# Performance work log

Measured on AMD Instinct MI355X. Metric: run time of the kernel, lower is better.

Reference implementation:

```python
import jax, jax.numpy as jnp
import numpy as np

B, S, D, H = 2, 2048, 2048, 16
DEPTH = D // H


def setup_inputs() -> dict:
    key = jax.random.key(0)
    ks = jax.random.split(key, 12)
    std = 1.0 / np.sqrt(D)
    mk = lambda k, shape: (jax.random.uniform(k, shape, jnp.float32) * 2 - 1) * std
    # causal additive mask: 1.0 where future position (masked), 0.0 elsewhere
    mask = jnp.triu(jnp.ones((S, S), jnp.float32), k=1)[None, None]
    return {
        "q": jax.random.normal(ks[0], (B, S, D), jnp.float32),
        "k": jax.random.normal(ks[1], (B, S, D), jnp.float32),
        "v": jax.random.normal(ks[2], (B, S, D), jnp.float32),
        "mask": mask,
        "wq_w": mk(ks[3], (D, D)), "wq_b": mk(ks[4], (D,)),
        "wk_w": mk(ks[5], (D, D)), "wk_b": mk(ks[6], (D,)),
        "wv_w": mk(ks[7], (D, D)), "wv_b": mk(ks[8], (D,)),
        "dense_w": mk(ks[9], (D, D)), "dense_b": mk(ks[10], (D,)),
    }


def split_heads(x):
    # [B,S,D] -> [B,H,S,depth]
    b, s, _ = x.shape
    return x.reshape(b, s, H, DEPTH).transpose(0, 2, 1, 3)


def reference(q, k, v, mask, wq_w, wq_b, wk_w, wk_b, wv_w, wv_b, dense_w, dense_b):
    # torch Linear: y = x @ W.T + b
    qh = split_heads(q @ wq_w.T + wq_b)
    kh = split_heads(k @ wk_w.T + wk_b)
    vh = split_heads(v @ wv_w.T + wv_b)
    scale = 1.0 / jnp.sqrt(jnp.asarray(DEPTH, jnp.float32))
    logits = jnp.einsum("bhqd,bhkd->bhqk", qh, kh) * scale
    logits = logits + mask * (-1e9)
    weights = jax.nn.softmax(logits, axis=-1)  # dropout is identity in eval
    out = jnp.einsum("bhqk,bhkd->bhqd", weights, vh)
    out = out.transpose(0, 2, 1, 3).reshape(q.shape[0], -1, D)
    return out @ dense_w.T + dense_b
```

## Files before the change

kernel.cpp:

```cpp
#include <hip/hip_runtime.h>
#include <hip/hip_bf16.h>


typedef __bf16 bf16x8 __attribute__((ext_vector_type(8)));
typedef float f32x4 __attribute__((ext_vector_type(4)));
typedef float f32x16 __attribute__((ext_vector_type(16)));
typedef unsigned short u16;
typedef unsigned int u32;

#define DEV static __device__ __forceinline__

DEV void gload_lds16(const void* g, void* l) {
  __builtin_amdgcn_global_load_lds(
      (const __attribute__((address_space(1))) void*)g,
      (__attribute__((address_space(3))) void*)l, 16, 0, 0);
}

DEV f32x4 mfma16(bf16x8 a, bf16x8 b, f32x4 c) {
  return __builtin_amdgcn_mfma_f32_16x16x32_bf16(a, b, c, 0, 0, 0);
}

DEV f32x16 mfma32(bf16x8 a, bf16x8 b, f32x16 c) {
  return __builtin_amdgcn_mfma_f32_32x32x16_bf16(a, b, c, 0, 0, 0);
}

DEV u16 f2bf(float x) {
  return __builtin_bit_cast(u16, __float2bfloat16(x));
}

DEV u32 pack2(float lo, float hi_) {
  return (u32)f2bf(lo) | ((u32)f2bf(hi_) << 16);
}

#define BAR() __builtin_amdgcn_s_barrier()

__global__ void __launch_bounds__(256) conv_f32_bf16(
    const float* __restrict__ in, u16* __restrict__ out) {
  const size_t i = ((size_t)blockIdx.x * 256 + threadIdx.x) * 4;
  const float4 v = *reinterpret_cast<const float4*>(in + i);
  ushort4 o;
  o.x = f2bf(v.x); o.y = f2bf(v.y); o.z = f2bf(v.z); o.w = f2bf(v.w);
  *reinterpret_cast<ushort4*>(out + i) = o;
}

__global__ void __launch_bounds__(256) conv_all(
    const float* __restrict__ s0, const float* __restrict__ s1,
    const float* __restrict__ s2, const float* __restrict__ s3,
    const float* __restrict__ s4, const float* __restrict__ s5,
    const float* __restrict__ s6,
    u16* __restrict__ d0, u16* __restrict__ d1, u16* __restrict__ d2,
    u16* __restrict__ d3, u16* __restrict__ d4, u16* __restrict__ d5,
    u16* __restrict__ d6, const size_t nact, const size_t nw) {
  const int j = blockIdx.y;
  const size_t i = ((size_t)blockIdx.x * 256 + threadIdx.x) * 4;
  const float* s; u16* d; size_t n;
  switch (j) {
    case 0: s = s0; d = d0; n = nact; break;
    case 1: s = s1; d = d1; n = nact; break;
    case 2: s = s2; d = d2; n = nact; break;
    case 3: s = s3; d = d3; n = nw; break;
    case 4: s = s4; d = d4; n = nw; break;
    case 5: s = s5; d = d5; n = nw; break;
    default: s = s6; d = d6; n = nw; break;
  }
  if (i >= n) return;
  const float4 v = *reinterpret_cast<const float4*>(s + i);
  ushort4 o;
  o.x = f2bf(v.x); o.y = f2bf(v.y); o.z = f2bf(v.z); o.w = f2bf(v.w);
  *reinterpret_cast<ushort4*>(d + i) = o;
}

#define GK 2048

DEV void gemm128_core(const u16* __restrict__ A, const u16* __restrict__ Bw,
                      const float* __restrict__ bias, void* __restrict__ Cout,
                      const int m0, const int n0, const int N,
                      const int out_f32, u16* AsB, u16* BsB) {
  const int tid = threadIdx.x;
  const int lane = tid & 63;
  const int wid = tid >> 6;
  const int wr = wid >> 1, wc = wid & 1;
  const int g = lane >> 4;
  const int r16 = lane & 15;

  int offA[2], offB[2], dstE[2];
#pragma unroll
  for (int rr = 0; rr < 2; ++rr) {
    const int G = rr * 256 + tid;
    const int rp = G >> 3;
    const int s = (G & 7) ^ (rp & 7);
    const int row = rp * 2 + (s >> 2);
    const int ch = s & 3;
    offA[rr] = (m0 + row) * GK + ch * 8;
    offB[rr] = (n0 + row) * GK + ch * 8;
    dstE[rr] = rr * 2048 + wid * 512;
  }

#define STAGE_A(kt, kh) do {                                              \
    u16* base_ = AsB + (((kt) & 1) * 2 + (kh)) * 4096;                    \
    const int go_ = (kt) * 64 + (kh) * 32;                                \
    gload_lds16(A + (size_t)(offA[0] + go_), base_ + dstE[0]);            \
    gload_lds16(A + (size_t)(offA[1] + go_), base_ + dstE[1]);            \
  } while (0)
#define STAGE_B(kt, kh) do {                                              \
    u16* base_ = BsB + (((kt) & 1) * 2 + (kh)) * 4096;                    \
    const int go_ = (kt) * 64 + (kh) * 32;                                \
    gload_lds16(Bw + (size_t)(offB[0] + go_), base_ + dstE[0]);           \
    gload_lds16(Bw + (size_t)(offB[1] + go_), base_ + dstE[1]);           \
  } while (0)
#define READ_A2(MH, buf) do {                                             \
    _Pragma("unroll") for (int i_ = 0; i_ < 2; ++i_) {                    \
      const int row_ = wr * 64 + ((MH) * 2 + i_) * 16 + r16;              \
      const int rp_ = row_ >> 1;                                          \
      const int sl_ = (((row_ & 1) << 2) | g) ^ (rp_ & 7);                \
      const int off_ = rp_ * 64 + sl_ * 8;                                \
      af[i_][0] = *(const bf16x8*)(AsB + ((buf) * 2 + 0) * 4096 + off_);  \
      af[i_][1] = *(const bf16x8*)(AsB + ((buf) * 2 + 1) * 4096 + off_);  \
    } } while (0)
#define READ_B4(buf) do {                                                 \
    _Pragma("unroll") for (int j_ = 0; j_ < 4; ++j_) {                    \
      const int row_ = wc * 64 + j_ * 16 + r16;                           \
      const int rp_ = row_ >> 1;                                          \
      const int sl_ = (((row_ & 1) << 2) | g) ^ (rp_ & 7);                \
      const int off_ = rp_ * 64 + sl_ * 8;                                \
      bf[j_][0] = *(const bf16x8*)(BsB + ((buf) * 2 + 0) * 4096 + off_);  \
      bf[j_][1] = *(const bf16x8*)(BsB + ((buf) * 2 + 1) * 4096 + off_);  \
    } } while (0)
#define MFMA16(MH) do {                                                   \
    __builtin_amdgcn_s_setprio(1);                                        \
    _Pragma("unroll") for (int i_ = 0; i_ < 2; ++i_)                      \
    _Pragma("unroll") for (int j_ = 0; j_ < 4; ++j_) {                    \
      f32x4 c_ = acc[(MH) * 2 + i_][j_];                                  \
      c_ = mfma16(af[i_][0], bf[j_][0], c_);                              \
      c_ = mfma16(af[i_][1], bf[j_][1], c_);                              \
      acc[(MH) * 2 + i_][j_] = c_;                                        \
    }                                                                     \
    __builtin_amdgcn_s_setprio(0);                                        \
  } while (0)

  f32x4 acc[4][4];
#pragma unroll
  for (int i = 0; i < 4; ++i)
#pragma unroll
    for (int j = 0; j < 4; ++j) acc[i][j] = {0.f, 0.f, 0.f, 0.f};

  bf16x8 af[2][2], bf[4][2];

  STAGE_B(0, 0); STAGE_B(0, 1); STAGE_A(0, 0); STAGE_A(0, 1);
  STAGE_B(1, 0); STAGE_B(1, 1);
  asm volatile("s_waitcnt vmcnt(4)" ::: "memory");
  BAR();

  for (int it = 0; it < 16; ++it) {
    const bool tail = (it == 15);
    const int T = 2 * it;
    const int b0 = T & 1, b1 = (T + 1) & 1;
    READ_A2(0, b0); READ_B4(b0);
    STAGE_A(T + 1, 0); STAGE_A(T + 1, 1);
    BAR(); MFMA16(0); BAR();
    READ_A2(1, b0);
    if (!tail) {
      STAGE_B(T + 2, 0); STAGE_B(T + 2, 1);
      asm volatile("s_waitcnt vmcnt(4)" ::: "memory");
    } else {
      asm volatile("s_waitcnt vmcnt(0)" ::: "memory");
    }
    BAR(); MFMA16(1); BAR();
    READ_A2(0, b1); READ_B4(b1);
    if (!tail) { STAGE_A(T + 2, 0); STAGE_A(T + 2, 1); }
    BAR(); MFMA16(0); BAR();
    READ_A2(1, b1);
    if (!tail) {
      STAGE_B(T + 3, 0); STAGE_B(T + 3, 1);
      asm volatile("s_waitcnt vmcnt(4)" ::: "memory");
    } else {
      asm volatile("s_waitcnt vmcnt(0)" ::: "memory");
    }
    BAR(); MFMA16(1); BAR();
  }

  const int rbase = m0 + wr * 64 + g * 4;
  const int cb = n0 + wc * 64 + r16;
#pragma unroll
  for (int i = 0; i < 4; ++i) {
#pragma unroll
    for (int j = 0; j < 4; ++j) {
      const int c = cb + j * 16;
      const float bv = bias[c];
#pragma unroll
      for (int r = 0; r < 4; ++r) {
        const float v = acc[i][j][r] + bv;
        const size_t idx = (size_t)(rbase + i * 16 + r) * N + c;
        if (out_f32) ((float*)Cout)[idx] = v;
        else ((u16*)Cout)[idx] = f2bf(v);
      }
    }
  }
#undef STAGE_A
#undef STAGE_B
#undef READ_A2
#undef READ_B4
#undef MFMA16
}

__global__ void __launch_bounds__(256, 2) gemm_qkv3(
    const u16* __restrict__ A0, const u16* __restrict__ A1,
    const u16* __restrict__ A2, const u16* __restrict__ W0,
    const u16* __restrict__ W1, const u16* __restrict__ W2,
    const float* __restrict__ b0, const float* __restrict__ b1,
    const float* __restrict__ b2, u16* __restrict__ C0,
    u16* __restrict__ C1, u16* __restrict__ C2) {
  __shared__ u16 AsB[4 * 4096];
  __shared__ u16 BsB[4 * 4096];
  const int xcd = blockIdx.x & 7;
  const int t = blockIdx.x >> 3;
  const int which = t >> 6;
  const int r = t & 63;
  const int m0 = (xcd * 4 + (r >> 4)) << 7;
  const int n0 = (r & 15) << 7;
  const u16* A = which == 0 ? A0 : which == 1 ? A1 : A2;
  const u16* W = which == 0 ? W0 : which == 1 ? W1 : W2;
  const float* bb = which == 0 ? b0 : which == 1 ? b1 : b2;
  u16* C = which == 0 ? C0 : which == 1 ? C1 : C2;
  gemm128_core(A, W, bb, C, m0, n0, 2048, 0, AsB, BsB);
}

__global__ void __launch_bounds__(256, 2) gemm_one(
    const u16* __restrict__ A, const u16* __restrict__ Bw,
    const float* __restrict__ bias, void* __restrict__ Cout,
    const int out_f32) {
  __shared__ u16 AsB[4 * 4096];
  __shared__ u16 BsB[4 * 4096];
  const int xcd = blockIdx.x & 7;
  const int t = blockIdx.x >> 3;
  const int m0 = (xcd * 4 + (t >> 4)) << 7;
  const int n0 = (t & 15) << 7;
  gemm128_core(A, Bw, bias, Cout, m0, n0, 2048, out_f32, AsB, BsB);
}

#define SEQ 2048
#define DMODEL 2048
#define DH 128
#define QBLK 128
#define KBLK 64
#define C1 0.12751744f
#define THR_RAW 62.73f

__global__ void __launch_bounds__(256, 2) flash_attn(
    const u16* __restrict__ Qh, const u16* __restrict__ Kh,
    const u16* __restrict__ Vh, u16* __restrict__ O) {
  __shared__ u16 Ks[2][KBLK * DH];
  __shared__ u16 Vt[DH * KBLK];

  const int tid = threadIdx.x;
  const int lane = tid & 63;
  const int w = tid >> 6;
  const int hi = lane >> 5;
  const int l31 = lane & 31;

  const int cc = blockIdx.x;
  const int low = cc & 15;
  const int bh = (cc >> 4) & 31;
  const int h = bh & 15;
  const int b = bh >> 4;
  const int g0 = low ^ h;
  const int qt = b ? (15 - g0) : g0;
  const int q0 = qt * QBLK;
  const size_t rowbase = (size_t)b * SEQ;
  const int hoff = h * DH;
  const int qw = q0 + w * 32;
  const int qlane = qw + l31;

  bf16x8 aq[8];
  {
    const u16* qp = &Qh[(rowbase + qlane) * DMODEL + hoff + hi * 8];
#pragma unroll
    for (int c = 0; c < 8; ++c)
      aq[c] = *reinterpret_cast<const bf16x8*>(qp + c * 16);
  }

  f32x16 oacc[4];
#pragma unroll
  for (int dt = 0; dt < 4; ++dt)
#pragma unroll
    for (int r = 0; r < 16; ++r) oacc[dt][r] = 0.f;
  float mrow = -1e30f, lrow = 0.f;

  const int krl = w * 16 + (lane >> 4);
  const int kg4 = w * 4 + (lane >> 4);
  const int du = lane & 15;

  const int nkt = 2 * qt + 2;
  const int ktd = qw >> 6;

  auto stageK = [&](int kt) {
#pragma unroll
    for (int i = 0; i < 4; ++i) {
      const int r = krl + i * 4;
      const int cg = (lane & 15) ^ (r & 15);
      gload_lds16(&Kh[(rowbase + kt * KBLK + r) * DMODEL + hoff + cg * 8],
                  &Ks[kt & 1][(w * 16 + i * 4) * DH]);
    }
  };

  stageK(0);
  uint4 vv[4];
#pragma unroll
  for (int r = 0; r < 4; ++r)
    vv[r] = *reinterpret_cast<const uint4*>(
        &Vh[(rowbase + kg4 * 4 + r) * DMODEL + hoff + du * 8]);

  for (int kt = 0; kt < nkt; ++kt) {
    const int k0 = kt * KBLK;
    if (kt + 1 < nkt) {
      stageK(kt + 1);
      asm volatile("s_waitcnt vmcnt(4)" ::: "memory");
    } else {
      asm volatile("s_waitcnt vmcnt(0)" ::: "memory");
    }

#pragma unroll
    for (int j = 0; j < 8; ++j) {
      const int d = du * 8 + j;
      ushort4 pk4;
      pk4.x = ((const u16*)&vv[0])[j];
      pk4.y = ((const u16*)&vv[1])[j];
      pk4.z = ((const u16*)&vv[2])[j];
      pk4.w = ((const u16*)&vv[3])[j];
      const int slot = (((kg4 >> 1) ^ ((d >> 2) & 7)) * 8) + (kg4 & 1) * 4;
      *reinterpret_cast<ushort4*>(&Vt[d * KBLK + slot]) = pk4;
    }
    asm volatile("s_waitcnt lgkmcnt(0)" ::: "memory");
    BAR();

    const bool active = (kt <= ktd);
    const u16* kb = &Ks[kt & 1][0];
    float p[2][16];
    bool act1 = false;

    if (active) {
      const bool diag = (kt == ktd);
      act1 = (kt < ktd) || (w & 1);
      const bool m0q = diag && !(w & 1);
      const bool m1q = diag && (w & 1);
      {
        f32x16 s;
#pragma unroll
        for (int r = 0; r < 16; ++r) s[r] = 0.f;
        __builtin_amdgcn_s_setprio(1);
#pragma unroll
        for (int c = 0; c < 8; ++c) {
          const int row = l31;
          const bf16x8 kf = *reinterpret_cast<const bf16x8*>(
              &kb[row * DH + (((c * 2 + hi) ^ (row & 15)) * 8)]);
          s = mfma32(kf, aq[c], s);
        }
        __builtin_amdgcn_s_setprio(0);
#pragma unroll
        for (int r = 0; r < 16; ++r) {
          const int krow = (r & 3) + 8 * (r >> 2) + 4 * hi;
          p[0][r] = (m0q && (k0 + krow > qlane)) ? -1e9f : s[r];
        }
      }
      if (act1) {
        f32x16 s;
#pragma unroll
        for (int r = 0; r < 16; ++r) s[r] = 0.f;
        __builtin_amdgcn_s_setprio(1);
#pragma unroll
        for (int c = 0; c < 8; ++c) {
          const int row = 32 + l31;
          const bf16x8 kf = *reinterpret_cast<const bf16x8*>(
              &kb[row * DH + (((c * 2 + hi) ^ (row & 15)) * 8)]);
          s = mfma32(kf, aq[c], s);
        }
        __builtin_amdgcn_s_setprio(0);
#pragma unroll
        for (int r = 0; r < 16; ++r) {
          const int krow = (r & 3) + 8 * (r >> 2) + 4 * hi;
          p[1][r] = (m1q && (k0 + 32 + krow > qlane)) ? -1e9f : s[r];
        }
      } else {
#pragma unroll
        for (int r = 0; r < 16; ++r) p[1][r] = -1e9f;
      }
    }

    if (kt + 1 < nkt) {
#pragma unroll
      for (int r = 0; r < 4; ++r)
        vv[r] = *reinterpret_cast<const uint4*>(
            &Vh[(rowbase + k0 + KBLK + kg4 * 4 + r) * DMODEL + hoff + du * 8]);
    }

    if (active) {
      float mx0 = fmaxf(p[0][0], p[1][0]);
      float mx1 = fmaxf(p[0][1], p[1][1]);
      float mx2 = fmaxf(p[0][2], p[1][2]);
      float mx3 = fmaxf(p[0][3], p[1][3]);
#pragma unroll
      for (int r = 4; r < 16; r += 4) {
        mx0 = fmaxf(mx0, fmaxf(p[0][r + 0], p[1][r + 0]));
        mx1 = fmaxf(mx1, fmaxf(p[0][r + 1], p[1][r + 1]));
        mx2 = fmaxf(mx2, fmaxf(p[0][r + 2], p[1][r + 2]));
        mx3 = fmaxf(mx3, fmaxf(p[0][r + 3], p[1][r + 3]));
      }
      float mx = fmaxf(fmaxf(mx0, mx1), fmaxf(mx2, mx3));
      mx = fmaxf(mx, __shfl_xor(mx, 32));

      const bool need = (mx > mrow + THR_RAW);
      if (__any((int)need)) {
        const float mn = fmaxf(mrow, mx);
        const float al = exp2f((mrow - mn) * C1);
        mrow = mn;
        lrow *= al;
#pragma unroll
        for (int r = 0; r < 16; ++r) {
          const float ar = __shfl(al, (r & 3) + 8 * (r >> 2) + 4 * hi);
#pragma unroll
          for (int dt = 0; dt < 4; ++dt) oacc[dt][r] *= ar;
        }
      }

      float s0 = 0.f, s1 = 0.f, s2 = 0.f, s3 = 0.f;
#pragma unroll
      for (int t = 0; t < 2; ++t)
#pragma unroll
        for (int r = 0; r < 16; r += 4) {
          p[t][r + 0] = exp2f((p[t][r + 0] - mrow) * C1);
          p[t][r + 1] = exp2f((p[t][r + 1] - mrow) * C1);
          p[t][r + 2] = exp2f((p[t][r + 2] - mrow) * C1);
          p[t][r + 3] = exp2f((p[t][r + 3] - mrow) * C1);
          s0 += p[t][r + 0]; s1 += p[t][r + 1];
          s2 += p[t][r + 2]; s3 += p[t][r + 3];
        }
      float sum = (s0 + s1) + (s2 + s3);
      sum += __shfl_xor(sum, 32);
      lrow += sum;

      u32 pk[2][8];
#pragma unroll
      for (int t = 0; t < 2; ++t)
#pragma unroll
        for (int m = 0; m < 8; ++m)
          pk[t][m] = pack2(p[t][2 * m], p[t][2 * m + 1]);

      __builtin_amdgcn_s_setprio(1);
#pragma unroll
      for (int ks = 0; ks < 4; ++ks) {
        if (ks >= 2 && !act1) break;
        const int t = ks >> 1;
        const int bs = (ks & 1) * 4;
        const u32 q0s = __shfl_xor(pk[t][bs + 0], 32);
        const u32 q1s = __shfl_xor(pk[t][bs + 1], 32);
        const u32 q2s = __shfl_xor(pk[t][bs + 2], 32);
        const u32 q3s = __shfl_xor(pk[t][bs + 3], 32);
        union { u32 u[4]; bf16x8 v; } pa;
        pa.u[0] = hi ? q2s : pk[t][bs + 0];
        pa.u[1] = hi ? q3s : pk[t][bs + 1];
        pa.u[2] = hi ? pk[t][bs + 2] : q0s;
        pa.u[3] = hi ? pk[t][bs + 3] : q1s;
#pragma unroll
        for (int dt = 0; dt < 4; ++dt) {
          const int d = dt * 32 + l31;
          const bf16x8 vf = *reinterpret_cast<const bf16x8*>(
              &Vt[d * KBLK + (((ks * 2 + hi) ^ ((d >> 2) & 7)) * 8)]);
          oacc[dt] = mfma32(pa.v, vf, oacc[dt]);
        }
      }
      __builtin_amdgcn_s_setprio(0);
    }

    BAR();
  }

  const float li = __builtin_amdgcn_rcpf(lrow);
#pragma unroll
  for (int r = 0; r < 16; ++r) {
    const int rowq = (r & 3) + 8 * (r >> 2) + 4 * hi;
    const float lr = __shfl(li, rowq);
    u16* op = &O[(rowbase + qw + rowq) * DMODEL + hoff + l31];
#pragma unroll
    for (int dt = 0; dt < 4; ++dt) op[dt * 32] = f2bf(oacc[dt][r] * lr);
  }
}

extern "C" void kernel_launch(void* const* d_in, const int* in_sizes, int n_in,
                              void* d_out, int out_size, void* d_ws,
                              size_t ws_size, hipStream_t stream) {
  const int Bv = 2, S = 2048, D = 2048;
  const int M = Bv * S;
  const size_t NT = (size_t)M * D;
  const size_t NW = (size_t)D * D;

  const float* q = (const float*)d_in[0];
  const float* k = (const float*)d_in[1];
  const float* v = (const float*)d_in[2];
  const float* wq_w = (const float*)d_in[4];
  const float* wq_b = (const float*)d_in[5];
  const float* wk_w = (const float*)d_in[6];
  const float* wk_b = (const float*)d_in[7];
  const float* wv_w = (const float*)d_in[8];
  const float* wv_b = (const float*)d_in[9];
  const float* dw = (const float*)d_in[10];
  const float* db = (const float*)d_in[11];
  float* out = (float*)d_out;

  const dim3 blk(256);
  const dim3 gattn(512);
  const size_t need = (7 * NT + 4 * NW) * 2;

  if (ws_size >= need) {
    u16* base = (u16*)d_ws;
    u16* Xq = base;
    u16* Xk = Xq + NT;
    u16* Xv = Xk + NT;
    u16* Wq = Xv + NT;
    u16* Wk = Wq + NW;
    u16* Wv = Wk + NW;
    u16* Wd = Wv + NW;
    u16* Qh = Wd + NW;
    u16* Kh = Qh + NT;
    u16* Vh = Kh + NT;
    u16* Obf = Vh + NT;

    conv_all<<<dim3((unsigned)(NT / 1024), 7), blk, 0, stream>>>(
        q, k, v, wq_w, wk_w, wv_w, dw, Xq, Xk, Xv, Wq, Wk, Wv, Wd, NT, NW);
    gemm_qkv3<<<dim3(1536), blk, 0, stream>>>(
        Xq, Xk, Xv, Wq, Wk, Wv, wq_b, wk_b, wv_b, Qh, Kh, Vh);
    flash_attn<<<gattn, blk, 0, stream>>>(Qh, Kh, Vh, Obf);
    gemm_one<<<dim3(512), blk, 0, stream>>>(Obf, Wd, db, out, 1);
  } else {
    u16* Xbf = (u16*)d_ws;
    u16* Wbf = Xbf + NT;
    u16* Qh = Wbf + NW;
    u16* Kh = Qh + NT;
    u16* Vh = Kh + NT;
    u16* Obf = Vh + NT;
    const dim3 gact((unsigned)(NT / 1024));
    const dim3 gw((unsigned)(NW / 1024));

    conv_f32_bf16<<<gact, blk, 0, stream>>>(q, Xbf);
    conv_f32_bf16<<<gw, blk, 0, stream>>>(wq_w, Wbf);
    gemm_one<<<dim3(512), blk, 0, stream>>>(Xbf, Wbf, wq_b, Qh, 0);
    conv_f32_bf16<<<gact, blk, 0, stream>>>(k, Xbf);
    conv_f32_bf16<<<gw, blk, 0, stream>>>(wk_w, Wbf);
    gemm_one<<<dim3(512), blk, 0, stream>>>(Xbf, Wbf, wk_b, Kh, 0);
    conv_f32_bf16<<<gact, blk, 0, stream>>>(v, Xbf);
    conv_f32_bf16<<<gw, blk, 0, stream>>>(wv_w, Wbf);
    gemm_one<<<dim3(512), blk, 0, stream>>>(Xbf, Wbf, wv_b, Vh, 0);
    flash_attn<<<gattn, blk, 0, stream>>>(Qh, Kh, Vh, Obf);
    conv_f32_bf16<<<gw, blk, 0, stream>>>(dw, Wbf);
    gemm_one<<<dim3(512), blk, 0, stream>>>(Obf, Wbf, db, out, 1);
  }
}
```

Baseline: 289.4 us.

## Use persistent flash-attention blocks with atomic work queue, longest jobs first

Turns the attention kernel into a persistent kernel: 768 blocks repeatedly take job indices from a global atomic counter, ordered so the longest causal query tiles (most key tiles) are handed out first. Occupancy hint rises from 2 to 3 blocks per CU. The aim is to balance the triangular causal workload across CUs and cut the tail imbalance. In exchange it adds an atomic plus a barrier per job, a memset launch, and extra register pressure from the higher occupancy target.

```diff
diff --git a/kernel.cpp b/kernel.cpp
--- a/kernel.cpp
+++ b/kernel.cpp
@@ -243,14 +243,17 @@
 #define DH 128
 #define QBLK 128
 #define KBLK 64
+#define NJOBS 512
 #define C1 0.12751744f
 #define THR_RAW 62.73f
 
-__global__ void __launch_bounds__(256, 2) flash_attn(
+__global__ void __launch_bounds__(256, 3) flash_attn(
     const u16* __restrict__ Qh, const u16* __restrict__ Kh,
-    const u16* __restrict__ Vh, u16* __restrict__ O) {
+    const u16* __restrict__ Vh, u16* __restrict__ O,
+    u32* __restrict__ ctr) {
   __shared__ u16 Ks[2][KBLK * DH];
   __shared__ u16 Vt[DH * KBLK];
+  __shared__ int s_job;
 
   const int tid = threadIdx.x;
   const int lane = tid & 63;
@@ -258,230 +261,235 @@
   const int hi = lane >> 5;
   const int l31 = lane & 31;
 
-  const int cc = blockIdx.x;
-  const int low = cc & 15;
-  const int bh = (cc >> 4) & 31;
-  const int h = bh & 15;
-  const int b = bh >> 4;
-  const int g0 = low ^ h;
-  const int qt = b ? (15 - g0) : g0;
-  const int q0 = qt * QBLK;
-  const size_t rowbase = (size_t)b * SEQ;
-  const int hoff = h * DH;
-  const int qw = q0 + w * 32;
-  const int qlane = qw + l31;
-
-  bf16x8 aq[8];
-  {
-    const u16* qp = &Qh[(rowbase + qlane) * DMODEL + hoff + hi * 8];
-#pragma unroll
-    for (int c = 0; c < 8; ++c)
-      aq[c] = *reinterpret_cast<const bf16x8*>(qp + c * 16);
-  }
-
-  f32x16 oacc[4];
-#pragma unroll
-  for (int dt = 0; dt < 4; ++dt)
-#pragma unroll
-    for (int r = 0; r < 16; ++r) oacc[dt][r] = 0.f;
-  float mrow = -1e30f, lrow = 0.f;
-
   const int krl = w * 16 + (lane >> 4);
   const int kg4 = w * 4 + (lane >> 4);
   const int du = lane & 15;
 
-  const int nkt = 2 * qt + 2;
-  const int ktd = qw >> 6;
-
-  auto stageK = [&](int kt) {
-#pragma unroll
-    for (int i = 0; i < 4; ++i) {
-      const int r = krl + i * 4;
-      const int cg = (lane & 15) ^ (r & 15);
-      gload_lds16(&Kh[(rowbase + kt * KBLK + r) * DMODEL + hoff + cg * 8],
-                  &Ks[kt & 1][(w * 16 + i * 4) * DH]);
+  for (;;) {
+    if (tid == 0) s_job = (int)atomicAdd(ctr, 1u);
+    __syncthreads();
+    const int job = s_job;
+    if (job >= NJOBS) return;
+
+    const int qt = 15 - (job >> 5);
+    const int bh = job & 31;
+    const int h = bh & 15;
+    const int b = bh >> 4;
+    const int q0 = qt * QBLK;
+    const size_t rowbase = (size_t)b * SEQ;
+    const int hoff = h * DH;
+    const int qw = q0 + w * 32;
+    const int qlane = qw + l31;
+
+    bf16x8 aq[8];
+    {
+      const u16* qp = &Qh[(rowbase + qlane) * DMODEL + hoff + hi * 8];
+#pragma unroll
+      for (int c = 0; c < 8; ++c)
+        aq[c] = *reinterpret_cast<const bf16x8*>(qp + c * 16);
     }
-  };
-
-  stageK(0);
-  uint4 vv[4];
-#pragma unroll
-  for (int r = 0; r < 4; ++r)
-    vv[r] = *reinterpret_cast<const uint4*>(
-        &Vh[(rowbase + kg4 * 4 + r) * DMODEL + hoff + du * 8]);
-
-  for (int kt = 0; kt < nkt; ++kt) {
-    const int k0 = kt * KBLK;
-    if (kt + 1 < nkt) {
-      stageK(kt + 1);
-      asm volatile("s_waitcnt vmcnt(4)" ::: "memory");
-    } else {
-      asm volatile("s_waitcnt vmcnt(0)" ::: "memory");
-    }
-
-#pragma unroll
-    for (int j = 0; j < 8; ++j) {
-      const int d = du * 8 + j;
-      ushort4 pk4;
-      pk4.x = ((const u16*)&vv[0])[j];
-      pk4.y = ((const u16*)&vv[1])[j];
-      pk4.z = ((const u16*)&vv[2])[j];
-      pk4.w = ((const u16*)&vv[3])[j];
-      const int slot = (((kg4 >> 1) ^ ((d >> 2) & 7)) * 8) + (kg4 & 1) * 4;
-      *reinterpret_cast<ushort4*>(&Vt[d * KBLK + slot]) = pk4;
-    }
-    asm volatile("s_waitcnt lgkmcnt(0)" ::: "memory");
-    BAR();
-
-    const bool active = (kt <= ktd);
-    const u16* kb = &Ks[kt & 1][0];
-    float p[2][16];
-    bool act1 = false;
-
-    if (active) {
-      const bool diag = (kt == ktd);
-      act1 = (kt < ktd) || (w & 1);
-      const bool m0q = diag && !(w & 1);
-      const bool m1q = diag && (w & 1);
-      {
-        f32x16 s;
-#pragma unroll
-        for (int r = 0; r < 16; ++r) s[r] = 0.f;
+
+    f32x16 oacc[4];
+#pragma unroll
+    for (int dt = 0; dt < 4; ++dt)
+#pragma unroll
+      for (int r = 0; r < 16; ++r) oacc[dt][r] = 0.f;
+    float mrow = -1e30f, lrow = 0.f;
+
+    const int nkt = 2 * qt + 2;
+    const int ktd = qw >> 6;
+
+    auto stageK = [&](int kt) {
+#pragma unroll
+      for (int i = 0; i < 4; ++i) {
+        const int r = krl + i * 4;
+        const int cg = (lane & 15) ^ (r & 15);
+        gload_lds16(&Kh[(rowbase + kt * KBLK + r) * DMODEL + hoff + cg * 8],
+                    &Ks[kt & 1][(w * 16 + i * 4) * DH]);
+      }
+    };
+
+    stageK(0);
+    uint4 vv[4];
+#pragma unroll
+    for (int r = 0; r < 4; ++r)
+      vv[r] = *reinterpret_cast<const uint4*>(
+          &Vh[(rowbase + kg4 * 4 + r) * DMODEL + hoff + du * 8]);
+
+    for (int kt = 0; kt < nkt; ++kt) {
+      const int k0 = kt * KBLK;
+      if (kt + 1 < nkt) {
+        stageK(kt + 1);
+        asm volatile("s_waitcnt vmcnt(4)" ::: "memory");
+      } else {
+        asm volatile("s_waitcnt vmcnt(0)" ::: "memory");
+      }
+
+#pragma unroll
+      for (int j = 0; j < 8; ++j) {
+        const int d = du * 8 + j;
+        ushort4 pk4;
+        pk4.x = ((const u16*)&vv[0])[j];
+        pk4.y = ((const u16*)&vv[1])[j];
+        pk4.z = ((const u16*)&vv[2])[j];
+        pk4.w = ((const u16*)&vv[3])[j];
+        const int slot = (((kg4 >> 1) ^ ((d >> 2) & 7)) * 8) + (kg4 & 1) * 4;
+        *reinterpret_cast<ushort4*>(&Vt[d * KBLK + slot]) = pk4;
+      }
+      asm volatile("s_waitcnt lgkmcnt(0)" ::: "memory");
+      BAR();
+
+      const bool active = (kt <= ktd);
+      const u16* kb = &Ks[kt & 1][0];
+      float p[2][16];
+      bool act1 = false;
+
+      if (active) {
+        const bool diag = (kt == ktd);
+        act1 = (kt < ktd) || (w & 1);
+        const bool m0q = diag && !(w & 1);
+        const bool m1q = diag && (w & 1);
+        {
+          f32x16 s;
+#pragma unroll
+          for (int r = 0; r < 16; ++r) s[r] = 0.f;
+          __builtin_amdgcn_s_setprio(1);
+#pragma unroll
+          for (int c = 0; c < 8; ++c) {
+            const int row = l31;
+            const bf16x8 kf = *reinterpret_cast<const bf16x8*>(
+                &kb[row * DH + (((c * 2 + hi) ^ (row & 15)) * 8)]);
+            s = mfma32(kf, aq[c], s);
+          }
+          __builtin_amdgcn_s_setprio(0);
+#pragma unroll
+          for (int r = 0; r < 16; ++r) {
+            const int krow = (r & 3) + 8 * (r >> 2) + 4 * hi;
+            p[0][r] = (m0q && (k0 + krow > qlane)) ? -1e9f : s[r];
+          }
+        }
+        if (act1) {
+          f32x16 s;
+#pragma unroll
+          for (int r = 0; r < 16; ++r) s[r] = 0.f;
+          __builtin_amdgcn_s_setprio(1);
+#pragma unroll
+          for (int c = 0; c < 8; ++c) {
+            const int row = 32 + l31;
+            const bf16x8 kf = *reinterpret_cast<const bf16x8*>(
+                &kb[row * DH + (((c * 2 + hi) ^ (row & 15)) * 8)]);
+            s = mfma32(kf, aq[c], s);
+          }
+          __builtin_amdgcn_s_setprio(0);
+#pragma unroll
+          for (int r = 0; r < 16; ++r) {
+            const int krow = (r & 3) + 8 * (r >> 2) + 4 * hi;
+            p[1][r] = (m1q && (k0 + 32 + krow > qlane)) ? -1e9f : s[r];
+          }
+        } else {
+#pragma unroll
+          for (int r = 0; r < 16; ++r) p[1][r] = -1e9f;
+        }
+      }
+
+      if (kt + 1 < nkt) {
+#pragma unroll
+        for (int r = 0; r < 4; ++r)
+          vv[r] = *reinterpret_cast<const uint4*>(
+              &Vh[(rowbase + k0 + KBLK + kg4 * 4 + r) * DMODEL + hoff +
+                  du * 8]);
+      }
+
+      if (active) {
+        float mx0 = fmaxf(p[0][0], p[1][0]);
+        float mx1 = fmaxf(p[0][1], p[1][1]);
+        float mx2 = fmaxf(p[0][2], p[1][2]);
+        float mx3 = fmaxf(p[0][3], p[1][3]);
+#pragma unroll
+        for (int r = 4; r < 16; r += 4) {
+          mx0 = fmaxf(mx0, fmaxf(p[0][r + 0], p[1][r + 0]));
+          mx1 = fmaxf(mx1, fmaxf(p[0][r + 1], p[1][r + 1]));
+          mx2 = fmaxf(mx2, fmaxf(p[0][r + 2], p[1][r + 2]));
+          mx3 = fmaxf(mx3, fmaxf(p[0][r + 3], p[1][r + 3]));
+        }
+        float mx = fmaxf(fmaxf(mx0, mx1), fmaxf(mx2, mx3));
+        mx = fmaxf(mx, __shfl_xor(mx, 32));
+
+        const bool need = (mx > mrow + THR_RAW);
+        if (__any((int)need)) {
+          const float mn = fmaxf(mrow, mx);
+          const float al = exp2f((mrow - mn) * C1);
+          mrow = mn;
+          lrow *= al;
+#pragma unroll
+          for (int r = 0; r < 16; ++r) {
+            const float ar = __shfl(al, (r & 3) + 8 * (r >> 2) + 4 * hi);
+#pragma unroll
+            for (int dt = 0; dt < 4; ++dt) oacc[dt][r] *= ar;
+          }
+        }
+
+        float s0 = 0.f, s1 = 0.f, s2 = 0.f, s3 = 0.f;
+#pragma unroll
+        for (int t = 0; t < 2; ++t)
+#pragma unroll
+          for (int r = 0; r < 16; r += 4) {
+            p[t][r + 0] = exp2f((p[t][r + 0] - mrow) * C1);
+            p[t][r + 1] = exp2f((p[t][r + 1] - mrow) * C1);
+            p[t][r + 2] = exp2f((p[t][r + 2] - mrow) * C1);
+            p[t][r + 3] = exp2f((p[t][r + 3] - mrow) * C1);
+            s0 += p[t][r + 0]; s1 += p[t][r + 1];
+            s2 += p[t][r + 2]; s3 += p[t][r + 3];
+          }
+        float sum = (s0 + s1) + (s2 + s3);
+        sum += __shfl_xor(sum, 32);
+        lrow += sum;
+
+        u32 pk[2][8];
+#pragma unroll
+        for (int t = 0; t < 2; ++t)
+#pragma unroll
+          for (int m = 0; m < 8; ++m)
+            pk[t][m] = pack2(p[t][2 * m], p[t][2 * m + 1]);
+
         __builtin_amdgcn_s_setprio(1);
 #pragma unroll
-        for (int c = 0; c < 8; ++c) {
-          const int row = l31;
-          const bf16x8 kf = *reinterpret_cast<const bf16x8*>(
-              &kb[row * DH + (((c * 2 + hi) ^ (row & 15)) * 8)]);
-          s = mfma32(kf, aq[c], s);
+        for (int ks = 0; ks < 4; ++ks) {
+          if (ks >= 2 && !act1) break;
+          const int t = ks >> 1;
+          const int bs = (ks & 1) * 4;
+          const u32 q0s = __shfl_xor(pk[t][bs + 0], 32);
+          const u32 q1s = __shfl_xor(pk[t][bs + 1], 32);
+          const u32 q2s = __shfl_xor(pk[t][bs + 2], 32);
+          const u32 q3s = __shfl_xor(pk[t][bs + 3], 32);
+          union { u32 u[4]; bf16x8 v; } pa;
+          pa.u[0] = hi ? q2s : pk[t][bs + 0];
+          pa.u[1] = hi ? q3s : pk[t][bs + 1];
+          pa.u[2] = hi ? pk[t][bs + 2] : q0s;
+          pa.u[3] = hi ? pk[t][bs + 3] : q1s;
+#pragma unroll
+          for (int dt = 0; dt < 4; ++dt) {
+            const int d = dt * 32 + l31;
+            const bf16x8 vf = *reinterpret_cast<const bf16x8*>(
+                &Vt[d * KBLK + (((ks * 2 + hi) ^ ((d >> 2) & 7)) * 8)]);
+            oacc[dt] = mfma32(pa.v, vf, oacc[dt]);
+          }
         }
         __builtin_amdgcn_s_setprio(0);
-#pragma unroll
-        for (int r = 0; r < 16; ++r) {
-          const int krow = (r & 3) + 8 * (r >> 2) + 4 * hi;
-          p[0][r] = (m0q && (k0 + krow > qlane)) ? -1e9f : s[r];
-        }
-      }
-      if (act1) {
-        f32x16 s;
-#pragma unroll
-        for (int r = 0; r < 16; ++r) s[r] = 0.f;
-        __builtin_amdgcn_s_setprio(1);
-#pragma unroll
-        for (int c = 0; c < 8; ++c) {
-          const int row = 32 + l31;
-          const bf16x8 kf = *reinterpret_cast<const bf16x8*>(
-              &kb[row * DH + (((c * 2 + hi) ^ (row & 15)) * 8)]);
-          s = mfma32(kf, aq[c], s);
-        }
-        __builtin_amdgcn_s_setprio(0);
-#pragma unroll
-        for (int r = 0; r < 16; ++r) {
-          const int krow = (r & 3) + 8 * (r >> 2) + 4 * hi;
-          p[1][r] = (m1q && (k0 + 32 + krow > qlane)) ? -1e9f : s[r];
-        }
-      } else {
-#pragma unroll
-        for (int r = 0; r < 16; ++r) p[1][r] = -1e9f;
-      }
+      }
+
+      BAR();
     }
 
-    if (kt + 1 < nkt) {
-#pragma unroll
-      for (int r = 0; r < 4; ++r)
-        vv[r] = *reinterpret_cast<const uint4*>(
-            &Vh[(rowbase + k0 + KBLK + kg4 * 4 + r) * DMODEL + hoff + du * 8]);
+    const float li = __builtin_amdgcn_rcpf(lrow);
+#pragma unroll
+    for (int r = 0; r < 16; ++r) {
+      const int rowq = (r & 3) + 8 * (r >> 2) + 4 * hi;
+      const float lr = __shfl(li, rowq);
+      u16* op = &O[(rowbase + qw + rowq) * DMODEL + hoff + l31];
+#pragma unroll
+      for (int dt = 0; dt < 4; ++dt) op[dt * 32] = f2bf(oacc[dt][r] * lr);
     }
-
-    if (active) {
-      float mx0 = fmaxf(p[0][0], p[1][0]);
-      float mx1 = fmaxf(p[0][1], p[1][1]);
-      float mx2 = fmaxf(p[0][2], p[1][2]);
-      float mx3 = fmaxf(p[0][3], p[1][3]);
-#pragma unroll
-      for (int r = 4; r < 16; r += 4) {
-        mx0 = fmaxf(mx0, fmaxf(p[0][r + 0], p[1][r + 0]));
-        mx1 = fmaxf(mx1, fmaxf(p[0][r + 1], p[1][r + 1]));
-        mx2 = fmaxf(mx2, fmaxf(p[0][r + 2], p[1][r + 2]));
-        mx3 = fmaxf(mx3, fmaxf(p[0][r + 3], p[1][r + 3]));
-      }
-      float mx = fmaxf(fmaxf(mx0, mx1), fmaxf(mx2, mx3));
-      mx = fmaxf(mx, __shfl_xor(mx, 32));
-
-      const bool need = (mx > mrow + THR_RAW);
-      if (__any((int)need)) {
-        const float mn = fmaxf(mrow, mx);
-        const float al = exp2f((mrow - mn) * C1);
-        mrow = mn;
-        lrow *= al;
-#pragma unroll
-        for (int r = 0; r < 16; ++r) {
-          const float ar = __shfl(al, (r & 3) + 8 * (r >> 2) + 4 * hi);
-#pragma unroll
-          for (int dt = 0; dt < 4; ++dt) oacc[dt][r] *= ar;
-        }
-      }
-
-      float s0 = 0.f, s1 = 0.f, s2 = 0.f, s3 = 0.f;
-#pragma unroll
-      for (int t = 0; t < 2; ++t)
-#pragma unroll
-        for (int r = 0; r < 16; r += 4) {
-          p[t][r + 0] = exp2f((p[t][r + 0] - mrow) * C1);
-          p[t][r + 1] = exp2f((p[t][r + 1] - mrow) * C1);
-          p[t][r + 2] = exp2f((p[t][r + 2] - mrow) * C1);
-          p[t][r + 3] = exp2f((p[t][r + 3] - mrow) * C1);
-          s0 += p[t][r + 0]; s1 += p[t][r + 1];
-          s2 += p[t][r + 2]; s3 += p[t][r + 3];
-        }
-      float sum = (s0 + s1) + (s2 + s3);
-      sum += __shfl_xor(sum, 32);
-      lrow += sum;
-
-      u32 pk[2][8];
-#pragma unroll
-      for (int t = 0; t < 2; ++t)
-#pragma unroll
-        for (int m = 0; m < 8; ++m)
-          pk[t][m] = pack2(p[t][2 * m], p[t][2 * m + 1]);
-
-      __builtin_amdgcn_s_setprio(1);
-#pragma unroll
-      for (int ks = 0; ks < 4; ++ks) {
-        if (ks >= 2 && !act1) break;
-        const int t = ks >> 1;
-        const int bs = (ks & 1) * 4;
-        const u32 q0s = __shfl_xor(pk[t][bs + 0], 32);
-        const u32 q1s = __shfl_xor(pk[t][bs + 1], 32);
-        const u32 q2s = __shfl_xor(pk[t][bs + 2], 32);
-        const u32 q3s = __shfl_xor(pk[t][bs + 3], 32);
-        union { u32 u[4]; bf16x8 v; } pa;
-        pa.u[0] = hi ? q2s : pk[t][bs + 0];
-        pa.u[1] = hi ? q3s : pk[t][bs + 1];
-        pa.u[2] = hi ? pk[t][bs + 2] : q0s;
-        pa.u[3] = hi ? pk[t][bs + 3] : q1s;
-#pragma unroll
-        for (int dt = 0; dt < 4; ++dt) {
-          const int d = dt * 32 + l31;
-          const bf16x8 vf = *reinterpret_cast<const bf16x8*>(
-              &Vt[d * KBLK + (((ks * 2 + hi) ^ ((d >> 2) & 7)) * 8)]);
-          oacc[dt] = mfma32(pa.v, vf, oacc[dt]);
-        }
-      }
-      __builtin_amdgcn_s_setprio(0);
-    }
-
-    BAR();
-  }
-
-  const float li = __builtin_amdgcn_rcpf(lrow);
-#pragma unroll
-  for (int r = 0; r < 16; ++r) {
-    const int rowq = (r & 3) + 8 * (r >> 2) + 4 * hi;
-    const float lr = __shfl(li, rowq);
-    u16* op = &O[(rowbase + qw + rowq) * DMODEL + hoff + l31];
-#pragma unroll
-    for (int dt = 0; dt < 4; ++dt) op[dt * 32] = f2bf(oacc[dt][r] * lr);
   }
 }
 
@@ -507,8 +515,8 @@
   float* out = (float*)d_out;
 
   const dim3 blk(256);
-  const dim3 gattn(512);
-  const size_t need = (7 * NT + 4 * NW) * 2;
+  const dim3 gattn(768);
+  const size_t need = (7 * NT + 4 * NW) * 2 + 64;
 
   if (ws_size >= need) {
     u16* base = (u16*)d_ws;
@@ -523,12 +531,14 @@
     u16* Kh = Qh + NT;
     u16* Vh = Kh + NT;
     u16* Obf = Vh + NT;
-
+    u32* ctr = (u32*)(Obf + NT);
+
+    hipMemsetAsync(ctr, 0, 4, stream);
     conv_all<<<dim3((unsigned)(NT / 1024), 7), blk, 0, stream>>>(
         q, k, v, wq_w, wk_w, wv_w, dw, Xq, Xk, Xv, Wq, Wk, Wv, Wd, NT, NW);
     gemm_qkv3<<<dim3(1536), blk, 0, stream>>>(
         Xq, Xk, Xv, Wq, Wk, Wv, wq_b, wk_b, wv_b, Qh, Kh, Vh);
-    flash_attn<<<gattn, blk, 0, stream>>>(Qh, Kh, Vh, Obf);
+    flash_attn<<<gattn, blk, 0, stream>>>(Qh, Kh, Vh, Obf, ctr);
     gemm_one<<<dim3(512), blk, 0, stream>>>(Obf, Wd, db, out, 1);
   } else {
     u16* Xbf = (u16*)d_ws;
@@ -537,9 +547,11 @@
     u16* Kh = Qh + NT;
     u16* Vh = Kh + NT;
     u16* Obf = Vh + NT;
+    u32* ctr = (u32*)(Obf + NT);
     const dim3 gact((unsigned)(NT / 1024));
     const dim3 gw((unsigned)(NW / 1024));
 
+    hipMemsetAsync(ctr, 0, 4, stream);
     conv_f32_bf16<<<gact, blk, 0, stream>>>(q, Xbf);
     conv_f32_bf16<<<gw, blk, 0, stream>>>(wq_w, Wbf);
     gemm_one<<<dim3(512), blk, 0, stream>>>(Xbf, Wbf, wq_b, Qh, 0);
@@ -549,7 +561,7 @@
     conv_f32_bf16<<<gact, blk, 0, stream>>>(v, Xbf);
     conv_f32_bf16<<<gw, blk, 0, stream>>>(wv_w, Wbf);
     gemm_one<<<dim3(512), blk, 0, stream>>>(Xbf, Wbf, wv_b, Vh, 0);
-    flash_attn<<<gattn, blk, 0, stream>>>(Qh, Kh, Vh, Obf);
+    flash_attn<<<gattn, blk, 0, stream>>>(Qh, Kh, Vh, Obf, ctr);
     conv_f32_bf16<<<gw, blk, 0, stream>>>(dw, Wbf);
     gemm_one<<<dim3(512), blk, 0, stream>>>(Obf, Wbf, db, out, 1);
   }
```

New measurement: 438.5 us. +51.5%, slower.

## Split long causal query tiles across two KV halves and merge partials

Applied to the files above, without the earlier changes.

The flash-attention grid now gives each of the eight longest causal query tiles two blocks, each covering half of the KV range. Each of these blocks writes its unnormalised fp32 output plus its running max and sum to a scratch buffer placed over the dead Xq region. A new merge kernel rescales and combines the two halves into the bf16 output. The aim is to shorten the longest block in the causal triangle so work is spread more evenly across CUs. In exchange it adds an extra kernel launch and fp32 partial-result traffic, and the fallback path puts the scratch buffer past the existing workspace layout.

```diff
diff --git a/kernel.cpp b/kernel.cpp
--- a/kernel.cpp
+++ b/kernel.cpp
@@ -243,12 +243,14 @@
 #define DH 128
 #define QBLK 128
 #define KBLK 64
+#define PHALF 16640
 #define C1 0.12751744f
 #define THR_RAW 62.73f
 
 __global__ void __launch_bounds__(256, 2) flash_attn(
     const u16* __restrict__ Qh, const u16* __restrict__ Kh,
-    const u16* __restrict__ Vh, u16* __restrict__ O) {
+    const u16* __restrict__ Vh, u16* __restrict__ O,
+    float* __restrict__ Pbuf) {
   __shared__ u16 Ks[2][KBLK * DH];
   __shared__ u16 Vt[DH * KBLK];
 
@@ -258,13 +260,28 @@
   const int hi = lane >> 5;
   const int l31 = lane & 31;
 
-  const int cc = blockIdx.x;
-  const int low = cc & 15;
-  const int bh = (cc >> 4) & 31;
+  const int c = blockIdx.x;
+  int qt, bh, ktLo, ktHi, half;
+  bool split;
+  if (c < 512) {
+    split = true;
+    qt = 15 - (c >> 6);
+    half = (c >> 5) & 1;
+    bh = c & 31;
+    const int L = qt + 1;
+    ktLo = half * L;
+    ktHi = ktLo + L;
+  } else {
+    split = false;
+    half = 0;
+    const int i = c - 512;
+    qt = i >> 5;
+    bh = i & 31;
+    ktLo = 0;
+    ktHi = 2 * qt + 2;
+  }
   const int h = bh & 15;
   const int b = bh >> 4;
-  const int g0 = low ^ h;
-  const int qt = b ? (15 - g0) : g0;
   const int q0 = qt * QBLK;
   const size_t rowbase = (size_t)b * SEQ;
   const int hoff = h * DH;
@@ -275,8 +292,8 @@
   {
     const u16* qp = &Qh[(rowbase + qlane) * DMODEL + hoff + hi * 8];
 #pragma unroll
-    for (int c = 0; c < 8; ++c)
-      aq[c] = *reinterpret_cast<const bf16x8*>(qp + c * 16);
+    for (int cc = 0; cc < 8; ++cc)
+      aq[cc] = *reinterpret_cast<const bf16x8*>(qp + cc * 16);
   }
 
   f32x16 oacc[4];
@@ -290,7 +307,6 @@
   const int kg4 = w * 4 + (lane >> 4);
   const int du = lane & 15;
 
-  const int nkt = 2 * qt + 2;
   const int ktd = qw >> 6;
 
   auto stageK = [&](int kt) {
@@ -303,16 +319,16 @@
     }
   };
 
-  stageK(0);
+  stageK(ktLo);
   uint4 vv[4];
 #pragma unroll
   for (int r = 0; r < 4; ++r)
     vv[r] = *reinterpret_cast<const uint4*>(
-        &Vh[(rowbase + kg4 * 4 + r) * DMODEL + hoff + du * 8]);
-
-  for (int kt = 0; kt < nkt; ++kt) {
+        &Vh[(rowbase + ktLo * KBLK + kg4 * 4 + r) * DMODEL + hoff + du * 8]);
+
+  for (int kt = ktLo; kt < ktHi; ++kt) {
     const int k0 = kt * KBLK;
-    if (kt + 1 < nkt) {
+    if (kt + 1 < ktHi) {
       stageK(kt + 1);
       asm volatile("s_waitcnt vmcnt(4)" ::: "memory");
     } else {
@@ -349,11 +365,11 @@
         for (int r = 0; r < 16; ++r) s[r] = 0.f;
         __builtin_amdgcn_s_setprio(1);
 #pragma unroll
-        for (int c = 0; c < 8; ++c) {
+        for (int cc = 0; cc < 8; ++cc) {
           const int row = l31;
           const bf16x8 kf = *reinterpret_cast<const bf16x8*>(
-              &kb[row * DH + (((c * 2 + hi) ^ (row & 15)) * 8)]);
-          s = mfma32(kf, aq[c], s);
+              &kb[row * DH + (((cc * 2 + hi) ^ (row & 15)) * 8)]);
+          s = mfma32(kf, aq[cc], s);
         }
         __builtin_amdgcn_s_setprio(0);
 #pragma unroll
@@ -368,11 +384,11 @@
         for (int r = 0; r < 16; ++r) s[r] = 0.f;
         __builtin_amdgcn_s_setprio(1);
 #pragma unroll
-        for (int c = 0; c < 8; ++c) {
+        for (int cc = 0; cc < 8; ++cc) {
           const int row = 32 + l31;
           const bf16x8 kf = *reinterpret_cast<const bf16x8*>(
-              &kb[row * DH + (((c * 2 + hi) ^ (row & 15)) * 8)]);
-          s = mfma32(kf, aq[c], s);
+              &kb[row * DH + (((cc * 2 + hi) ^ (row & 15)) * 8)]);
+          s = mfma32(kf, aq[cc], s);
         }
         __builtin_amdgcn_s_setprio(0);
 #pragma unroll
@@ -386,11 +402,12 @@
       }
     }
 
-    if (kt + 1 < nkt) {
+    if (kt + 1 < ktHi) {
 #pragma unroll
       for (int r = 0; r < 4; ++r)
         vv[r] = *reinterpret_cast<const uint4*>(
-            &Vh[(rowbase + k0 + KBLK + kg4 * 4 + r) * DMODEL + hoff + du * 8]);
+            &Vh[(rowbase + k0 + KBLK + kg4 * 4 + r) * DMODEL + hoff +
+                du * 8]);
     }
 
     if (active) {
@@ -474,14 +491,62 @@
     BAR();
   }
 
-  const float li = __builtin_amdgcn_rcpf(lrow);
-#pragma unroll
-  for (int r = 0; r < 16; ++r) {
-    const int rowq = (r & 3) + 8 * (r >> 2) + 4 * hi;
-    const float lr = __shfl(li, rowq);
-    u16* op = &O[(rowbase + qw + rowq) * DMODEL + hoff + l31];
-#pragma unroll
-    for (int dt = 0; dt < 4; ++dt) op[dt * 32] = f2bf(oacc[dt][r] * lr);
+  if (!split) {
+    const float li = __builtin_amdgcn_rcpf(lrow);
+#pragma unroll
+    for (int r = 0; r < 16; ++r) {
+      const int rowq = (r & 3) + 8 * (r >> 2) + 4 * hi;
+      const float lr = __shfl(li, rowq);
+      u16* op = &O[(rowbase + qw + rowq) * DMODEL + hoff + l31];
+#pragma unroll
+      for (int dt = 0; dt < 4; ++dt) op[dt * 32] = f2bf(oacc[dt][r] * lr);
+    }
+  } else {
+    float* Pb = Pbuf + ((size_t)((((qt - 8) << 5) | bh) * 2 + half)) * PHALF;
+#pragma unroll
+    for (int r = 0; r < 16; ++r) {
+      const int rowq = (r & 3) + 8 * (r >> 2) + 4 * hi;
+      float* op = &Pb[(size_t)(w * 32 + rowq) * 128 + l31];
+#pragma unroll
+      for (int dt = 0; dt < 4; ++dt) op[dt * 32] = oacc[dt][r];
+    }
+    if (hi == 0) {
+      Pb[16384 + w * 32 + l31] = mrow;
+      Pb[16512 + w * 32 + l31] = lrow;
+    }
+  }
+}
+
+__global__ void __launch_bounds__(256) merge_split(
+    const float* __restrict__ Pbuf, u16* __restrict__ O) {
+  const int p = blockIdx.x;
+  const int qt = 8 + (p >> 5);
+  const int bh = p & 31;
+  const int h = bh & 15;
+  const int b = bh >> 4;
+  const float* P0 = Pbuf + (size_t)(p * 2 + 0) * PHALF;
+  const float* P1 = Pbuf + (size_t)(p * 2 + 1) * PHALF;
+  const int row = threadIdx.x >> 1;
+  const int d0 = (threadIdx.x & 1) * 64;
+  const float m0 = P0[16384 + row], m1 = P1[16384 + row];
+  const float l0 = P0[16512 + row], l1 = P1[16512 + row];
+  const float m = fmaxf(m0, m1);
+  const float a0 = exp2f((m0 - m) * C1);
+  const float a1 = exp2f((m1 - m) * C1);
+  const float li = 1.0f / (a0 * l0 + a1 * l1);
+  u16* orow = &O[((size_t)b * SEQ + qt * QBLK + row) * DMODEL + h * DH + d0];
+  const float* r0 = &P0[(size_t)row * 128 + d0];
+  const float* r1 = &P1[(size_t)row * 128 + d0];
+#pragma unroll
+  for (int d = 0; d < 64; d += 4) {
+    const f32x4 o0 = *reinterpret_cast<const f32x4*>(r0 + d);
+    const f32x4 o1 = *reinterpret_cast<const f32x4*>(r1 + d);
+    ushort4 s;
+    s.x = f2bf((a0 * o0[0] + a1 * o1[0]) * li);
+    s.y = f2bf((a0 * o0[1] + a1 * o1[1]) * li);
+    s.z = f2bf((a0 * o0[2] + a1 * o1[2]) * li);
+    s.w = f2bf((a0 * o0[3] + a1 * o1[3]) * li);
+    *reinterpret_cast<ushort4*>(orow + d) = s;
   }
 }
 
@@ -507,7 +572,7 @@
   float* out = (float*)d_out;
 
   const dim3 blk(256);
-  const dim3 gattn(512);
+  const dim3 gattn(768);
   const size_t need = (7 * NT + 4 * NW) * 2;
 
   if (ws_size >= need) {
@@ -523,12 +588,14 @@
     u16* Kh = Qh + NT;
     u16* Vh = Kh + NT;
     u16* Obf = Vh + NT;
+    float* Pbuf = (float*)Xq;
 
     conv_all<<<dim3((unsigned)(NT / 1024), 7), blk, 0, stream>>>(
         q, k, v, wq_w, wk_w, wv_w, dw, Xq, Xk, Xv, Wq, Wk, Wv, Wd, NT, NW);
     gemm_qkv3<<<dim3(1536), blk, 0, stream>>>(
         Xq, Xk, Xv, Wq, Wk, Wv, wq_b, wk_b, wv_b, Qh, Kh, Vh);
-    flash_attn<<<gattn, blk, 0, stream>>>(Qh, Kh, Vh, Obf);
+    flash_attn<<<gattn, blk, 0, stream>>>(Qh, Kh, Vh, Obf, Pbuf);
+    merge_split<<<dim3(256), blk, 0, stream>>>(Pbuf, Obf);
     gemm_one<<<dim3(512), blk, 0, stream>>>(Obf, Wd, db, out, 1);
   } else {
     u16* Xbf = (u16*)d_ws;
@@ -537,6 +604,7 @@
     u16* Kh = Qh + NT;
     u16* Vh = Kh + NT;
     u16* Obf = Vh + NT;
+    float* Pbuf = (float*)(Obf + NT);
     const dim3 gact((unsigned)(NT / 1024));
     const dim3 gw((unsigned)(NW / 1024));
 
@@ -549,7 +617,8 @@
     conv_f32_bf16<<<gact, blk, 0, stream>>>(v, Xbf);
     conv_f32_bf16<<<gw, blk, 0, stream>>>(wv_w, Wbf);
     gemm_one<<<dim3(512), blk, 0, stream>>>(Xbf, Wbf, wv_b, Vh, 0);
-    flash_attn<<<gattn, blk, 0, stream>>>(Qh, Kh, Vh, Obf);
+    flash_attn<<<gattn, blk, 0, stream>>>(Qh, Kh, Vh, Obf, Pbuf);
+    merge_split<<<dim3(256), blk, 0, stream>>>(Pbuf, Obf);
     conv_f32_bf16<<<gw, blk, 0, stream>>>(dw, Wbf);
     gemm_one<<<dim3(512), blk, 0, stream>>>(Obf, Wbf, db, out, 1);
   }
```

New measurement: 295.8 us. 1.02x slower.
